# Performance work log

Hardware: AMD Instinct MI355X
Metric: run time of the kernel (lower is better)

The kernel has to match this reference:

```python
import jax, jax.numpy as jnp
import numpy as np

B, S, H = 1, 2048, 4096
NH, NKV, HD = 32, 8, 128
GROUPS = NH // NKV
ROPE_THETA = 10000.0
QMAX = 127.0  # symmetric 8-bit fake quant
MASK_MIN = -1e9


def fake_quant(x, axis=-1):
    # dynamic symmetric uniform quantize->dequantize along `axis`
    s = jnp.max(jnp.abs(x), axis=axis, keepdims=True) / QMAX
    s = jnp.maximum(s, 1e-8)
    q = jnp.clip(jnp.round(x / s), -QMAX - 1.0, QMAX) * s
    return x + jax.lax.stop_gradient(q - x)  # straight-through


def quant_linear(x, W):
    # per-token act quant, per-output-channel weight quant; W is [out, in]
    return fake_quant(x, axis=-1) @ fake_quant(W, axis=-1).T


def rope_cos_sin(position_ids):
    inv_freq = 1.0 / (ROPE_THETA ** (jnp.arange(0, HD, 2, dtype=jnp.float32) / HD))
    freqs = position_ids.astype(jnp.float32)[:, :, None] * inv_freq[None, None, :]  # [B,S,HD/2]
    emb = jnp.concatenate([freqs, freqs], axis=-1)  # [B,S,HD]
    return jnp.cos(emb)[:, None], jnp.sin(emb)[:, None]  # [B,1,S,HD]


def rotate_half(x):
    x1, x2 = x[..., : HD // 2], x[..., HD // 2:]
    return jnp.concatenate([-x2, x1], axis=-1)


def setup_inputs() -> dict:
    key = jax.random.key(0)
    ks = jax.random.split(key, 6)
    hidden_states = jax.random.normal(ks[0], (B, S, H), jnp.float32)
    causal = jnp.where(jnp.arange(S)[None, :] <= jnp.arange(S)[:, None], 0.0, MASK_MIN)
    attention_mask = jnp.broadcast_to(causal, (B, 1, S, S)).astype(jnp.float32)
    position_ids = jnp.broadcast_to(jnp.arange(S, dtype=jnp.int64), (B, S))
    Wq = jax.random.normal(ks[1], (H, H), jnp.float32) * 0.02
    Wk = jax.random.normal(ks[2], (NKV * HD, H), jnp.float32) * 0.02
    Wv = jax.random.normal(ks[3], (NKV * HD, H), jnp.float32) * 0.02
    Wo = jax.random.normal(ks[4], (H, H), jnp.float32) * 0.02
    return {"hidden_states": hidden_states, "attention_mask": attention_mask,
            "position_ids": position_ids, "Wq": Wq, "Wk": Wk, "Wv": Wv, "Wo": Wo}


def reference(hidden_states, attention_mask, position_ids, Wq, Wk, Wv, Wo):
    bsz, q_len, _ = hidden_states.shape
    # quantized projections
    q = quant_linear(hidden_states, Wq).reshape(bsz, q_len, NH, HD).transpose(0, 2, 1, 3)
    k = quant_linear(hidden_states, Wk).reshape(bsz, q_len, NKV, HD).transpose(0, 2, 1, 3)
    v = quant_linear(hidden_states, Wv).reshape(bsz, q_len, NKV, HD).transpose(0, 2, 1, 3)
    # RoPE
    cos, sin = rope_cos_sin(position_ids)
    q = q * cos + rotate_half(q) * sin
    k = k * cos + rotate_half(k) * sin
    # GQA repeat
    k = jnp.repeat(k, GROUPS, axis=1)  # [B,NH,S,HD]
    v = jnp.repeat(v, GROUPS, axis=1)
    # quantized QK^T
    q = fake_quant(q, axis=-1)
    k = fake_quant(k, axis=-1)
    attn_weights = jnp.einsum("bhqd,bhkd->bhqk", q, k) / np.sqrt(HD).astype(np.float32)
    attn_weights = attn_weights + attention_mask
    attn_weights = jnp.maximum(attn_weights, jnp.finfo(attn_weights.dtype).min)
    p = jax.nn.softmax(attn_weights.astype(jnp.float32), axis=-1).astype(q.dtype)
    # quantized PV
    p = fake_quant(p, axis=-1)
    v = fake_quant(v, axis=-1)
    attn_output = jnp.einsum("bhqk,bhkd->bhqd", p, v)
    attn_output = attn_output.transpose(0, 2, 1, 3).reshape(bsz, q_len, H)
    return quant_linear(attn_output, Wo)
```

## Files before the change

### kernel.cpp

```cpp
#include <hip/hip_runtime.h>
#include <hip/hip_bf16.h>
#include <math.h>

#define S_LEN 2048
#define HDIM  4096
#define NH    32
#define NKV   8
#define HD    128
#define KVD   (NKV * HD)
#define QKVN  6144

typedef int   v4i  __attribute__((ext_vector_type(4)));
typedef int   v16i __attribute__((ext_vector_type(16)));
typedef float v4f  __attribute__((ext_vector_type(4)));
typedef short v8s  __attribute__((ext_vector_type(8)));

#define GLL16(g, l) \
  __builtin_amdgcn_global_load_lds((__attribute__((address_space(1))) void*)(g), \
                                   (__attribute__((address_space(3))) void*)(l), 16, 0, 0)

__device__ __forceinline__ short f32_bf16(float f) {
  unsigned u = __builtin_bit_cast(unsigned, f);
  u = (u + 0x7FFFu + ((u >> 16) & 1u)) >> 16;
  return (short)u;
}

__device__ __forceinline__ int quant1(float x, float inv) {
  float q = rintf(x * inv);
  q = fminf(fmaxf(q, -128.0f), 127.0f);
  return (int)q;
}

__global__ void k_rope_tables(float* __restrict__ ct, float* __restrict__ st) {
  int idx = blockIdx.x * 256 + threadIdx.x;
  if (idx >= S_LEN * 64) return;
  int s = idx >> 6, d = idx & 63;
  float ex = (float)(2 * d) * (1.0f / 128.0f);
  float inv = 1.0f / powf(10000.0f, ex);
  float f = (float)s * inv;
  ct[idx] = cosf(f);
  st[idx] = sinf(f);
}

__global__ __launch_bounds__(256) void k_quant_rows(const float* __restrict__ src,
                                                    signed char* __restrict__ dst,
                                                    float* __restrict__ scales) {
  int r = blockIdx.x;
  const float* x = src + (size_t)r * HDIM;
  int t = threadIdx.x;
  float4 v[4];
  float am = 0.f;
#pragma unroll
  for (int i = 0; i < 4; ++i) {
    v[i] = ((const float4*)x)[i * 256 + t];
    am = fmaxf(am, fmaxf(fmaxf(fabsf(v[i].x), fabsf(v[i].y)),
                         fmaxf(fabsf(v[i].z), fabsf(v[i].w))));
  }
#pragma unroll
  for (int m = 1; m < 64; m <<= 1) am = fmaxf(am, __shfl_xor(am, m));
  __shared__ float red[4];
  if ((t & 63) == 0) red[t >> 6] = am;
  __syncthreads();
  am = fmaxf(fmaxf(red[0], red[1]), fmaxf(red[2], red[3]));
  float s = fmaxf(am * (1.0f / 127.0f), 1e-8f);
  float inv = 1.0f / s;
  if (t == 0) scales[r] = s;
  int* out = (int*)(dst + (size_t)r * HDIM);
#pragma unroll
  for (int i = 0; i < 4; ++i) {
    unsigned p = (unsigned)(quant1(v[i].x, inv) & 255)
               | ((unsigned)(quant1(v[i].y, inv) & 255) << 8)
               | ((unsigned)(quant1(v[i].z, inv) & 255) << 16)
               | ((unsigned)(quant1(v[i].w, inv) & 255) << 24);
    out[i * 256 + t] = (int)p;
  }
}

__global__ __launch_bounds__(256, 3) void k_gemm32(const signed char* __restrict__ A,
                                                   const float* __restrict__ sa,
                                                   const signed char* __restrict__ B,
                                                   const float* __restrict__ sb,
                                                   float* __restrict__ C, int N) {
  const int K = HDIM;
  int total = gridDim.x * 16;
  int id = blockIdx.y * gridDim.x + blockIdx.x;
  int nper = total >> 3;
  int nid = (id & 7) * nper + (id >> 3);
  int m0 = (nid & 15) * 128;
  int n0 = (nid >> 4) * 128;

  int lane = threadIdx.x & 63, w = threadIdx.x >> 6;
  int wrb = (w >> 1) << 6;
  int wcb = (w & 1) << 6;
  __shared__ signed char Al[2][8192];
  __shared__ signed char Bl[2][8192];
  int srow = lane >> 2;
  int schunk = (((lane & 3) ^ ((lane >> 2) & 3)) << 4);

  auto stage = [&](int buf, int k0) {
#pragma unroll
    for (int i = 0; i < 2; ++i) {
      int idx = w * 2 + i;
      int row = idx * 16 + srow;
      GLL16(A + (size_t)(m0 + row) * K + k0 + schunk, &Al[buf][idx * 1024]);
      GLL16(B + (size_t)(n0 + row) * K + k0 + schunk, &Bl[buf][idx * 1024]);
    }
  };

  v16i acc[2][2];
#pragma unroll
  for (int mt = 0; mt < 2; ++mt)
#pragma unroll
    for (int nt = 0; nt < 2; ++nt)
#pragma unroll
      for (int r = 0; r < 16; ++r) acc[mt][nt][r] = 0;

  stage(0, 0);
  __syncthreads();
  const int nk = K / 64;
  for (int t = 0; t < nk; ++t) {
    int pb = t & 1;
    if (t + 1 < nk) stage(pb ^ 1, (t + 1) * 64);
    const signed char* Ab = &Al[pb][0];
    const signed char* Bb = &Bl[pb][0];
#pragma unroll
    for (int kc = 0; kc < 2; ++kc) {
      int coff = kc * 32 + ((lane >> 5) * 16);
      v4i af[2], bf[2];
#pragma unroll
      for (int mt = 0; mt < 2; ++mt) {
        int row = wrb + mt * 32 + (lane & 31);
        af[mt] = *(const v4i*)(Ab + row * 64 + (coff ^ ((row & 3) << 4)));
      }
#pragma unroll
      for (int nt = 0; nt < 2; ++nt) {
        int row = wcb + nt * 32 + (lane & 31);
        bf[nt] = *(const v4i*)(Bb + row * 64 + (coff ^ ((row & 3) << 4)));
      }
#pragma unroll
      for (int mt = 0; mt < 2; ++mt)
#pragma unroll
        for (int nt = 0; nt < 2; ++nt)
          acc[mt][nt] = __builtin_amdgcn_mfma_i32_32x32x32_i8(af[mt], bf[nt], acc[mt][nt], 0, 0, 0);
    }
    __syncthreads();
  }

  int cn = lane & 31, g4 = (lane >> 5) * 4;
#pragma unroll
  for (int mt = 0; mt < 2; ++mt)
#pragma unroll
    for (int nt = 0; nt < 2; ++nt) {
      int n = n0 + wcb + nt * 32 + cn;
      float sbn = sb[n];
#pragma unroll
      for (int r = 0; r < 16; ++r) {
        int m = m0 + wrb + mt * 32 + (r & 3) + 8 * (r >> 2) + g4;
        C[(size_t)m * N + n] = (float)acc[mt][nt][r] * sa[m] * sbn;
      }
    }
}

__global__ void k_rope_quant(const float* __restrict__ src, const float* __restrict__ ct,
                             const float* __restrict__ st, signed char* __restrict__ dst,
                             float* __restrict__ scales, int colbase) {
  int b = blockIdx.x;
  int hh = b >> 11;
  int s = b & (S_LEN - 1);
  int d = threadIdx.x;
  size_t base = (size_t)s * QKVN + colbase + (size_t)hh * HD;
  float x1 = src[base + d];
  float x2 = src[base + d + 64];
  float c = ct[(s << 6) + d], sn = st[(s << 6) + d];
  float o1 = x1 * c - x2 * sn;
  float o2 = x2 * c + x1 * sn;
  float am = fmaxf(fabsf(o1), fabsf(o2));
#pragma unroll
  for (int m = 1; m < 64; m <<= 1) am = fmaxf(am, __shfl_xor(am, m));
  float sc = fmaxf(am * (1.0f / 127.0f), 1e-8f);
  float inv = 1.0f / sc;
  if (d == 0) scales[hh * S_LEN + s] = sc;
  signed char* o = dst + ((size_t)hh * S_LEN + s) * HD;
  o[d] = (signed char)quant1(o1, inv);
  o[d + 64] = (signed char)quant1(o2, inv);
}

__global__ void k_quant_v(const float* __restrict__ src, short* __restrict__ vt,
                          float* __restrict__ sv) {
  int b = blockIdx.x;
  int hk = b >> 11;
  int s = b & (S_LEN - 1);
  int d = threadIdx.x;
  size_t base = (size_t)s * QKVN + 5120 + (size_t)hk * HD;
  float x1 = src[base + d];
  float x2 = src[base + d + 64];
  float am = fmaxf(fabsf(x1), fabsf(x2));
#pragma unroll
  for (int m = 1; m < 64; m <<= 1) am = fmaxf(am, __shfl_xor(am, m));
  float sc = fmaxf(am * (1.0f / 127.0f), 1e-8f);
  float inv = 1.0f / sc;
  if (d == 0) sv[hk * S_LEN + s] = sc;
  int q1i = quant1(x1, inv), q2i = quant1(x2, inv);
  size_t vb = (size_t)hk * HD * S_LEN;
  vt[vb + (size_t)d * S_LEN + s] = f32_bf16((float)q1i);
  vt[vb + (size_t)(d + 64) * S_LEN + s] = f32_bf16((float)q2i);
}

__global__ __launch_bounds__(256, 2) void k_attn(const signed char* __restrict__ qi8,
                                                 const float* __restrict__ sq,
                                                 const signed char* __restrict__ ki8,
                                                 const float* __restrict__ sk,
                                                 const short* __restrict__ vt,
                                                 const float* __restrict__ sv,
                                                 float* __restrict__ out) {
  int h = blockIdx.x;
  int qt = 31 - blockIdx.y;
  int hk = h >> 2;
  int lane = threadIdx.x & 63;
  int w = threadIdx.x >> 6;
  int q0 = qt * 64;
  int wrow0 = q0 + w * 16;

  __shared__ signed char Kl[2][8192];
  __shared__ short Vl[2][8192];
  __shared__ short wlds[4][1024];

  const signed char* qbase = qi8 + (size_t)h * S_LEN * HD;
  const signed char* kbase = ki8 + (size_t)hk * S_LEN * HD;
  const char* vbase = (const char*)(vt + (size_t)hk * HD * S_LEN);
  const float* skh = sk + hk * S_LEN;
  const float* svh = sv + hk * S_LEN;

  long aq[4];
  {
    const signed char* qrow = qbase + (size_t)(wrow0 + (lane & 15)) * HD + ((lane >> 4) * 8);
#pragma unroll
    for (int ks = 0; ks < 4; ++ks) aq[ks] = *(const long*)(qrow + ks * 32);
  }
  int crow = (lane >> 4) * 4;
  int ccol = lane & 15;
  float sq2[4];
#pragma unroll
  for (int r = 0; r < 4; ++r)
    sq2[r] = sq[h * S_LEN + wrow0 + crow + r] *
             (0.08838834764831843f * 1.4426950408889634f);

  int ntiles = qt + 1;
  int srow8 = lane >> 3;
  int schunk = (((lane & 7) ^ srow8) << 4);

  auto stageK = [&](int jt, int buf) {
    int j0 = jt * 64;
#pragma unroll
    for (int i = 0; i < 2; ++i) {
      int idx = w * 2 + i;
      int row = idx * 8 + srow8;
      GLL16(kbase + (size_t)(j0 + row) * HD + schunk, &Kl[buf][idx * 1024]);
    }
  };
  auto stageV = [&](int jt, int buf) {
    int j0 = jt * 64;
#pragma unroll
    for (int i = 0; i < 4; ++i) {
      int idx = w * 4 + i;
      int row = idx * 8 + srow8;
      GLL16(vbase + (size_t)row * (S_LEN * 2) + (size_t)j0 * 2 + schunk,
            (char*)&Vl[buf][0] + idx * 1024);
    }
  };

  float mrow[4] = {-3e38f, -3e38f, -3e38f, -3e38f};
  stageK(0, 0);
  __syncthreads();
  for (int jt = 0; jt < ntiles; ++jt) {
    int pb = jt & 1;
    if (jt + 1 < ntiles) stageK(jt + 1, pb ^ 1);
    const signed char* Kb = &Kl[pb][0];
#pragma unroll
    for (int nt = 0; nt < 4; ++nt) {
      int jr = nt * 16 + ccol;
      const signed char* kr = Kb + jr * 128;
      v4i acc = {0, 0, 0, 0};
#pragma unroll
      for (int ks = 0; ks < 4; ++ks) {
        long b = *(const long*)(kr + ((ks * 32 + ((lane >> 4) * 8)) ^ ((jr & 7) << 4)));
        acc = __builtin_amdgcn_mfma_i32_16x16x32_i8(aq[ks], b, acc, 0, 0, 0);
      }
      int j = jt * 64 + jr;
      float skj = skh[j];
      if (jt == ntiles - 1) {
#pragma unroll
        for (int r = 0; r < 4; ++r)
          if (j <= wrow0 + crow + r)
            mrow[r] = fmaxf(mrow[r], (float)acc[r] * sq2[r] * skj);
      } else {
#pragma unroll
        for (int r = 0; r < 4; ++r)
          mrow[r] = fmaxf(mrow[r], (float)acc[r] * sq2[r] * skj);
      }
    }
    __syncthreads();
  }
#pragma unroll
  for (int r = 0; r < 4; ++r) {
    float v = mrow[r];
    v = fmaxf(v, __shfl_xor(v, 1));
    v = fmaxf(v, __shfl_xor(v, 2));
    v = fmaxf(v, __shfl_xor(v, 4));
    v = fmaxf(v, __shfl_xor(v, 8));
    mrow[r] = v;
  }

  float Z[4] = {0.f, 0.f, 0.f, 0.f};
  v4f accp[8];
  v4f zf = {0.f, 0.f, 0.f, 0.f};
#pragma unroll
  for (int dt = 0; dt < 8; ++dt) accp[dt] = zf;

  stageK(0, 0);
  stageV(0, 0);
  __syncthreads();
  for (int jt = 0; jt < ntiles; ++jt) {
    int pb = jt & 1;
    if (jt + 1 < ntiles) {
      stageK(jt + 1, pb ^ 1);
      stageV(jt + 1, pb ^ 1);
    }
    const signed char* Kb = &Kl[pb][0];
#pragma unroll
    for (int nt = 0; nt < 4; ++nt) {
      int jr = nt * 16 + ccol;
      const signed char* kr = Kb + jr * 128;
      v4i acc = {0, 0, 0, 0};
#pragma unroll
      for (int ks = 0; ks < 4; ++ks) {
        long b = *(const long*)(kr + ((ks * 32 + ((lane >> 4) * 8)) ^ ((jr & 7) << 4)));
        acc = __builtin_amdgcn_mfma_i32_16x16x32_i8(aq[ks], b, acc, 0, 0, 0);
      }
      int j = jt * 64 + jr;
      float skj = skh[j];
      float svj = svh[j];
      if (jt == ntiles - 1) {
#pragma unroll
        for (int r = 0; r < 4; ++r) {
          int row = crow + r;
          float e = (j <= wrow0 + row)
                        ? exp2f((float)acc[r] * sq2[r] * skj - mrow[r]) : 0.f;
          Z[r] += e;
          float wv = rintf(127.0f * e) * svj;
          int idx = ((row << 6) | (nt * 16 + ccol)) ^ ((row & 7) << 3);
          wlds[w][idx] = f32_bf16(wv);
        }
      } else {
#pragma unroll
        for (int r = 0; r < 4; ++r) {
          int row = crow + r;
          float e = exp2f((float)acc[r] * sq2[r] * skj - mrow[r]);
          Z[r] += e;
          float wv = rintf(127.0f * e) * svj;
          int idx = ((row << 6) | (nt * 16 + ccol)) ^ ((row & 7) << 3);
          wlds[w][idx] = f32_bf16(wv);
        }
      }
    }
    const short* Vb = &Vl[pb][0];
#pragma unroll
    for (int ks2 = 0; ks2 < 2; ++ks2) {
      int bels = (((lane & 15) << 6) + ks2 * 32 + ((lane >> 4) * 8)) ^ ((lane & 7) << 3);
      v8s aw = *(const v8s*)&wlds[w][bels];
#pragma unroll
      for (int dt = 0; dt < 8; ++dt) {
        int d = dt * 16 + (lane & 15);
        int off = (ks2 * 64 + ((lane >> 4) << 4)) ^ ((d & 7) << 4);
        v8s bv = *(const v8s*)((const char*)Vb + d * 128 + off);
        accp[dt] = __builtin_amdgcn_mfma_f32_16x16x32_bf16(aw, bv, accp[dt], 0, 0, 0);
      }
    }
    __syncthreads();
  }

#pragma unroll
  for (int r = 0; r < 4; ++r) {
    float v = Z[r];
    v += __shfl_xor(v, 1);
    v += __shfl_xor(v, 2);
    v += __shfl_xor(v, 4);
    v += __shfl_xor(v, 8);
    Z[r] = 1.0f / (127.0f * v);
  }
#pragma unroll
  for (int dt = 0; dt < 8; ++dt)
#pragma unroll
    for (int r = 0; r < 4; ++r) {
      int i = wrow0 + crow + r;
      int d = dt * 16 + ccol;
      out[(size_t)i * HDIM + (size_t)h * HD + d] = accp[dt][r] * Z[r];
    }
}

extern "C" void kernel_launch(void* const* d_in, const int* in_sizes, int n_in,
                              void* d_out, int out_size, void* d_ws, size_t ws_size,
                              hipStream_t stream) {
  const float* x  = (const float*)d_in[0];
  const float* Wq = (const float*)d_in[3];
  const float* Wk = (const float*)d_in[4];
  const float* Wv = (const float*)d_in[5];
  const float* Wo = (const float*)d_in[6];

  char* p = (char*)d_ws;
  auto alloc = [&](size_t sz) { char* r = p; p += (sz + 255) & ~(size_t)255; return r; };
  signed char* QX   = (signed char*)alloc((size_t)S_LEN * HDIM);
  float* SX         = (float*)alloc(S_LEN * 4);
  signed char* WQKV = (signed char*)alloc((size_t)QKVN * HDIM);
  float* SQKV       = (float*)alloc(QKVN * 4);
  signed char* WOI  = (signed char*)alloc((size_t)HDIM * HDIM);
  float* SWO        = (float*)alloc(HDIM * 4);
  float* QKVF       = (float*)alloc((size_t)S_LEN * QKVN * 4);
  signed char* QI8  = (signed char*)alloc((size_t)NH * S_LEN * HD);
  float* SQ         = (float*)alloc(NH * S_LEN * 4);
  signed char* KI8  = (signed char*)alloc((size_t)NKV * S_LEN * HD);
  float* SK         = (float*)alloc(NKV * S_LEN * 4);
  short* VT         = (short*)alloc((size_t)NKV * HD * S_LEN * 2);
  float* SV         = (float*)alloc(NKV * S_LEN * 4);
  float* CT         = (float*)alloc(S_LEN * 64 * 4);
  float* ST         = (float*)alloc(S_LEN * 64 * 4);
  float* SA         = (float*)alloc(S_LEN * 4);
  float* ATTNF     = QKVF;
  signed char* AI8 = QX;

  k_rope_tables<<<(S_LEN * 64 + 255) / 256, 256, 0, stream>>>(CT, ST);

  k_quant_rows<<<S_LEN, 256, 0, stream>>>(x, QX, SX);
  k_quant_rows<<<HDIM, 256, 0, stream>>>(Wq, WQKV, SQKV);
  k_quant_rows<<<KVD, 256, 0, stream>>>(Wk, WQKV + (size_t)4096 * HDIM, SQKV + 4096);
  k_quant_rows<<<KVD, 256, 0, stream>>>(Wv, WQKV + (size_t)5120 * HDIM, SQKV + 5120);
  k_quant_rows<<<HDIM, 256, 0, stream>>>(Wo, WOI, SWO);

  k_gemm32<<<dim3(QKVN / 128, S_LEN / 128), 256, 0, stream>>>(QX, SX, WQKV, SQKV, QKVF, QKVN);

  k_rope_quant<<<NH * S_LEN, 64, 0, stream>>>(QKVF, CT, ST, QI8, SQ, 0);
  k_rope_quant<<<NKV * S_LEN, 64, 0, stream>>>(QKVF, CT, ST, KI8, SK, 4096);
  k_quant_v<<<NKV * S_LEN, 64, 0, stream>>>(QKVF, VT, SV);

  k_attn<<<dim3(NH, 32), 256, 0, stream>>>(QI8, SQ, KI8, SK, VT, SV, ATTNF);

  k_quant_rows<<<S_LEN, 256, 0, stream>>>(ATTNF, AI8, SA);
  k_gemm32<<<dim3(HDIM / 128, S_LEN / 128), 256, 0, stream>>>(AI8, SA, WOI, SWO,
                                                              (float*)d_out, HDIM);
}
```

Baseline: 494.5 us.

## Double query rows per attention block and reuse K/V tiles across two M-tiles

Each attention block now handles 128 query rows (32 per wave, two 16-row MFMA tiles), so every K and V tile staged into LDS and every K fragment read feeds two MFMA tiles, halving the grid. The QK MFMA operands are swapped so scores come out transposed, which lets per-key scales load as float4 and lets row reductions use only cross-group shuffles. Probabilities are packed with v_cvt_pk_bf16_f32 into 8-byte LDS stores. The cost is more registers per wave (two accumulator sets), fewer blocks for load balancing, and some wasted work on causal diagonal tiles.

```diff
diff --git a/kernel.cpp b/kernel.cpp
--- a/kernel.cpp
+++ b/kernel.cpp
@@ -23,6 +23,12 @@
   unsigned u = __builtin_bit_cast(unsigned, f);
   u = (u + 0x7FFFu + ((u >> 16) & 1u)) >> 16;
   return (short)u;
+}
+
+__device__ __forceinline__ unsigned cvt_pk_bf16(float a, float b) {
+  unsigned r;
+  asm("v_cvt_pk_bf16_f32 %0, %1, %2" : "=v"(r) : "v"(a), "v"(b));
+  return r;
 }
 
 __device__ __forceinline__ int quant1(float x, float inv) {
@@ -214,16 +220,19 @@
                                                  const float* __restrict__ sv,
                                                  float* __restrict__ out) {
   int h = blockIdx.x;
-  int qt = 31 - blockIdx.y;
+  int qt2 = 15 - blockIdx.y;
   int hk = h >> 2;
   int lane = threadIdx.x & 63;
   int w = threadIdx.x >> 6;
-  int q0 = qt * 64;
-  int wrow0 = q0 + w * 16;
+  int c = lane & 15, g = lane >> 4;
+  int swz = (c & 7) << 4;
+  int q0 = qt2 * 128;
+  int wrow0 = q0 + w * 32;
+  int ntiles = 2 * qt2 + 2;
 
   __shared__ signed char Kl[2][8192];
   __shared__ short Vl[2][8192];
-  __shared__ short wlds[4][1024];
+  __shared__ short wlds[4][2048];
 
   const signed char* qbase = qi8 + (size_t)h * S_LEN * HD;
   const signed char* kbase = ki8 + (size_t)hk * S_LEN * HD;
@@ -231,21 +240,18 @@
   const float* skh = sk + hk * S_LEN;
   const float* svh = sv + hk * S_LEN;
 
-  long aq[4];
-  {
-    const signed char* qrow = qbase + (size_t)(wrow0 + (lane & 15)) * HD + ((lane >> 4) * 8);
-#pragma unroll
-    for (int ks = 0; ks < 4; ++ks) aq[ks] = *(const long*)(qrow + ks * 32);
-  }
-  int crow = (lane >> 4) * 4;
-  int ccol = lane & 15;
-  float sq2[4];
-#pragma unroll
-  for (int r = 0; r < 4; ++r)
-    sq2[r] = sq[h * S_LEN + wrow0 + crow + r] *
-             (0.08838834764831843f * 1.4426950408889634f);
-
-  int ntiles = qt + 1;
+  long bq[2][4];
+  float sq2[2];
+#pragma unroll
+  for (int mt = 0; mt < 2; ++mt) {
+    const signed char* qrow = qbase + (size_t)(wrow0 + 16 * mt + c) * HD + 8 * g;
+#pragma unroll
+    for (int ks = 0; ks < 4; ++ks) bq[mt][ks] = *(const long*)(qrow + ks * 32);
+    sq2[mt] = sq[h * S_LEN + wrow0 + 16 * mt + c] *
+              (0.08838834764831843f * 1.4426950408889634f);
+  }
+  int row_q[2] = {wrow0 + c, wrow0 + 16 + c};
+
   int srow8 = lane >> 3;
   int schunk = (((lane & 7) ^ srow8) << 4);
 
@@ -269,133 +275,153 @@
     }
   };
 
-  float mrow[4] = {-3e38f, -3e38f, -3e38f, -3e38f};
+  float m_[2] = {-3e38f, -3e38f};
   stageK(0, 0);
   __syncthreads();
   for (int jt = 0; jt < ntiles; ++jt) {
+    int j0 = jt * 64;
     int pb = jt & 1;
     if (jt + 1 < ntiles) stageK(jt + 1, pb ^ 1);
     const signed char* Kb = &Kl[pb][0];
+    bool act[2] = {j0 <= wrow0 + 15, j0 <= wrow0 + 31};
+    bool msk = (jt >= ntiles - 2);
 #pragma unroll
     for (int nt = 0; nt < 4; ++nt) {
-      int jr = nt * 16 + ccol;
-      const signed char* kr = Kb + jr * 128;
-      v4i acc = {0, 0, 0, 0};
-#pragma unroll
-      for (int ks = 0; ks < 4; ++ks) {
-        long b = *(const long*)(kr + ((ks * 32 + ((lane >> 4) * 8)) ^ ((jr & 7) << 4)));
-        acc = __builtin_amdgcn_mfma_i32_16x16x32_i8(aq[ks], b, acc, 0, 0, 0);
-      }
-      int j = jt * 64 + jr;
-      float skj = skh[j];
-      if (jt == ntiles - 1) {
-#pragma unroll
-        for (int r = 0; r < 4; ++r)
-          if (j <= wrow0 + crow + r)
-            mrow[r] = fmaxf(mrow[r], (float)acc[r] * sq2[r] * skj);
-      } else {
-#pragma unroll
-        for (int r = 0; r < 4; ++r)
-          mrow[r] = fmaxf(mrow[r], (float)acc[r] * sq2[r] * skj);
+      long kf[4];
+#pragma unroll
+      for (int ks = 0; ks < 4; ++ks)
+        kf[ks] = *(const long*)(Kb + (nt * 16 + c) * 128 + ((8 * g + 32 * ks) ^ swz));
+      float4 sk4 = *(const float4*)(skh + j0 + nt * 16 + 4 * g);
+#pragma unroll
+      for (int mt = 0; mt < 2; ++mt) {
+        if (!act[mt]) continue;
+        v4i acc = {0, 0, 0, 0};
+#pragma unroll
+        for (int ks = 0; ks < 4; ++ks)
+          acc = __builtin_amdgcn_mfma_i32_16x16x32_i8(kf[ks], bq[mt][ks], acc, 0, 0, 0);
+        float s2 = sq2[mt];
+        if (msk) {
+#pragma unroll
+          for (int r = 0; r < 4; ++r) {
+            int j = j0 + nt * 16 + 4 * g + r;
+            if (j <= row_q[mt]) m_[mt] = fmaxf(m_[mt], (float)acc[r] * s2 * sk4[r]);
+          }
+        } else {
+#pragma unroll
+          for (int r = 0; r < 4; ++r)
+            m_[mt] = fmaxf(m_[mt], (float)acc[r] * s2 * sk4[r]);
+        }
       }
     }
     __syncthreads();
   }
 #pragma unroll
-  for (int r = 0; r < 4; ++r) {
-    float v = mrow[r];
-    v = fmaxf(v, __shfl_xor(v, 1));
-    v = fmaxf(v, __shfl_xor(v, 2));
-    v = fmaxf(v, __shfl_xor(v, 4));
-    v = fmaxf(v, __shfl_xor(v, 8));
-    mrow[r] = v;
-  }
-
-  float Z[4] = {0.f, 0.f, 0.f, 0.f};
-  v4f accp[8];
+  for (int mt = 0; mt < 2; ++mt) {
+    m_[mt] = fmaxf(m_[mt], __shfl_xor(m_[mt], 16));
+    m_[mt] = fmaxf(m_[mt], __shfl_xor(m_[mt], 32));
+  }
+
+  float Z_[2] = {0.f, 0.f};
+  v4f accp[2][8];
   v4f zf = {0.f, 0.f, 0.f, 0.f};
 #pragma unroll
-  for (int dt = 0; dt < 8; ++dt) accp[dt] = zf;
-
+  for (int mt = 0; mt < 2; ++mt)
+#pragma unroll
+    for (int dt = 0; dt < 8; ++dt) accp[mt][dt] = zf;
+
+  short* wb = &wlds[w][0];
   stageK(0, 0);
   stageV(0, 0);
   __syncthreads();
   for (int jt = 0; jt < ntiles; ++jt) {
+    int j0 = jt * 64;
     int pb = jt & 1;
     if (jt + 1 < ntiles) {
       stageK(jt + 1, pb ^ 1);
       stageV(jt + 1, pb ^ 1);
     }
     const signed char* Kb = &Kl[pb][0];
+    bool act[2] = {j0 <= wrow0 + 15, j0 <= wrow0 + 31};
+    bool msk = (jt >= ntiles - 2);
 #pragma unroll
     for (int nt = 0; nt < 4; ++nt) {
-      int jr = nt * 16 + ccol;
-      const signed char* kr = Kb + jr * 128;
-      v4i acc = {0, 0, 0, 0};
-#pragma unroll
-      for (int ks = 0; ks < 4; ++ks) {
-        long b = *(const long*)(kr + ((ks * 32 + ((lane >> 4) * 8)) ^ ((jr & 7) << 4)));
-        acc = __builtin_amdgcn_mfma_i32_16x16x32_i8(aq[ks], b, acc, 0, 0, 0);
-      }
-      int j = jt * 64 + jr;
-      float skj = skh[j];
-      float svj = svh[j];
-      if (jt == ntiles - 1) {
-#pragma unroll
-        for (int r = 0; r < 4; ++r) {
-          int row = crow + r;
-          float e = (j <= wrow0 + row)
-                        ? exp2f((float)acc[r] * sq2[r] * skj - mrow[r]) : 0.f;
-          Z[r] += e;
-          float wv = rintf(127.0f * e) * svj;
-          int idx = ((row << 6) | (nt * 16 + ccol)) ^ ((row & 7) << 3);
-          wlds[w][idx] = f32_bf16(wv);
+      long kf[4];
+#pragma unroll
+      for (int ks = 0; ks < 4; ++ks)
+        kf[ks] = *(const long*)(Kb + (nt * 16 + c) * 128 + ((8 * g + 32 * ks) ^ swz));
+      float4 sk4 = *(const float4*)(skh + j0 + nt * 16 + 4 * g);
+      float4 sv4 = *(const float4*)(svh + j0 + nt * 16 + 4 * g);
+#pragma unroll
+      for (int mt = 0; mt < 2; ++mt) {
+        if (!act[mt]) continue;
+        v4i acc = {0, 0, 0, 0};
+#pragma unroll
+        for (int ks = 0; ks < 4; ++ks)
+          acc = __builtin_amdgcn_mfma_i32_16x16x32_i8(kf[ks], bq[mt][ks], acc, 0, 0, 0);
+        float s2 = sq2[mt], mm = m_[mt];
+        float pw[4];
+        if (msk) {
+#pragma unroll
+          for (int r = 0; r < 4; ++r) {
+            int j = j0 + nt * 16 + 4 * g + r;
+            float e = (j <= row_q[mt]) ? exp2f((float)acc[r] * s2 * sk4[r] - mm) : 0.f;
+            Z_[mt] += e;
+            pw[r] = rintf(127.0f * e) * sv4[r];
+          }
+        } else {
+#pragma unroll
+          for (int r = 0; r < 4; ++r) {
+            float e = exp2f((float)acc[r] * s2 * sk4[r] - mm);
+            Z_[mt] += e;
+            pw[r] = rintf(127.0f * e) * sv4[r];
+          }
         }
-      } else {
-#pragma unroll
-        for (int r = 0; r < 4; ++r) {
-          int row = crow + r;
-          float e = exp2f((float)acc[r] * sq2[r] * skj - mrow[r]);
-          Z[r] += e;
-          float wv = rintf(127.0f * e) * svj;
-          int idx = ((row << 6) | (nt * 16 + ccol)) ^ ((row & 7) << 3);
-          wlds[w][idx] = f32_bf16(wv);
-        }
-      }
-    }
-    const short* Vb = &Vl[pb][0];
+        uint2 pk;
+        pk.x = cvt_pk_bf16(pw[0], pw[1]);
+        pk.y = cvt_pk_bf16(pw[2], pw[3]);
+        *(uint2*)((char*)wb + (16 * mt + c) * 128 + ((32 * nt + 8 * g) ^ swz)) = pk;
+      }
+    }
+    const char* Vb = (const char*)&Vl[pb][0];
 #pragma unroll
     for (int ks2 = 0; ks2 < 2; ++ks2) {
-      int bels = (((lane & 15) << 6) + ks2 * 32 + ((lane >> 4) * 8)) ^ ((lane & 7) << 3);
-      v8s aw = *(const v8s*)&wlds[w][bels];
+      int boff = (64 * ks2 + 16 * g) ^ swz;
+      v8s aw[2];
+#pragma unroll
+      for (int mt = 0; mt < 2; ++mt)
+        if (act[mt]) aw[mt] = *(const v8s*)((const char*)wb + (16 * mt + c) * 128 + boff);
 #pragma unroll
       for (int dt = 0; dt < 8; ++dt) {
-        int d = dt * 16 + (lane & 15);
-        int off = (ks2 * 64 + ((lane >> 4) << 4)) ^ ((d & 7) << 4);
-        v8s bv = *(const v8s*)((const char*)Vb + d * 128 + off);
-        accp[dt] = __builtin_amdgcn_mfma_f32_16x16x32_bf16(aw, bv, accp[dt], 0, 0, 0);
+        v8s bv = *(const v8s*)(Vb + (16 * dt + c) * 128 + boff);
+#pragma unroll
+        for (int mt = 0; mt < 2; ++mt)
+          if (act[mt])
+            accp[mt][dt] = __builtin_amdgcn_mfma_f32_16x16x32_bf16(aw[mt], bv, accp[mt][dt], 0, 0, 0);
       }
     }
     __syncthreads();
   }
 
-#pragma unroll
-  for (int r = 0; r < 4; ++r) {
-    float v = Z[r];
-    v += __shfl_xor(v, 1);
-    v += __shfl_xor(v, 2);
-    v += __shfl_xor(v, 4);
-    v += __shfl_xor(v, 8);
-    Z[r] = 1.0f / (127.0f * v);
-  }
-#pragma unroll
-  for (int dt = 0; dt < 8; ++dt)
-#pragma unroll
-    for (int r = 0; r < 4; ++r) {
-      int i = wrow0 + crow + r;
-      int d = dt * 16 + ccol;
-      out[(size_t)i * HDIM + (size_t)h * HD + d] = accp[dt][r] * Z[r];
-    }
+  float zr[2][4];
+#pragma unroll
+  for (int mt = 0; mt < 2; ++mt) {
+    float z = Z_[mt];
+    z += __shfl_xor(z, 16);
+    z += __shfl_xor(z, 32);
+    float zn = 1.0f / (127.0f * z);
+#pragma unroll
+    for (int r = 0; r < 4; ++r) zr[mt][r] = __shfl(zn, 4 * g + r);
+  }
+#pragma unroll
+  for (int mt = 0; mt < 2; ++mt)
+#pragma unroll
+    for (int dt = 0; dt < 8; ++dt)
+#pragma unroll
+      for (int r = 0; r < 4; ++r) {
+        int i = wrow0 + 16 * mt + 4 * g + r;
+        int d = dt * 16 + c;
+        out[(size_t)i * HDIM + (size_t)h * HD + d] = accp[mt][dt][r] * zr[mt][r];
+      }
 }
 
 extern "C" void kernel_launch(void* const* d_in, const int* in_sizes, int n_in,
@@ -442,7 +468,7 @@
   k_rope_quant<<<NKV * S_LEN, 64, 0, stream>>>(QKVF, CT, ST, KI8, SK, 4096);
   k_quant_v<<<NKV * S_LEN, 64, 0, stream>>>(QKVF, VT, SV);
 
-  k_attn<<<dim3(NH, 32), 256, 0, stream>>>(QI8, SQ, KI8, SK, VT, SV, ATTNF);
+  k_attn<<<dim3(NH, 16), 256, 0, stream>>>(QI8, SQ, KI8, SK, VT, SV, ATTNF);
 
   k_quant_rows<<<S_LEN, 256, 0, stream>>>(ATTNF, AI8, SA);
   k_gemm32<<<dim3(HDIM / 128, S_LEN / 128), 256, 0, stream>>>(AI8, SA, WOI, SWO,
```

Result: slower. 538.8 us (+9.0%).
